# Performance work log

Measured on AMD Instinct MI355X. Metric: run time of the kernel, lower is better.

## Reference

```python
import jax, jax.numpy as jnp
import numpy as np

DIMS = 1024
HEAD = 16
HEAD_DIM = DIMS // HEAD  # 64
BASE_THETA = 10000.0


def setup_inputs() -> dict:
    key = jax.random.key(0)
    ks = jax.random.split(key, 8)
    B, S = 2, 2048
    x = jax.random.normal(ks[0], (B, S, DIMS), dtype=jnp.float32)
    # causal additive mask (use -1e9 instead of -inf for finite grads)
    mask = jnp.where(jnp.tril(jnp.ones((S, S), dtype=bool)), 0.0, -1e9).astype(jnp.float32)
    init = 0.02
    Wq = jax.random.normal(ks[1], (DIMS, DIMS), dtype=jnp.float32) * init
    bq = jnp.zeros((DIMS,), dtype=jnp.float32)
    Wk = jax.random.normal(ks[2], (DIMS, DIMS), dtype=jnp.float32) * init  # no bias
    Wv = jax.random.normal(ks[3], (DIMS, DIMS), dtype=jnp.float32) * init
    bv = jnp.zeros((DIMS,), dtype=jnp.float32)
    Wo = jax.random.normal(ks[4], (DIMS, DIMS), dtype=jnp.float32) * init
    bo = jnp.zeros((DIMS,), dtype=jnp.float32)
    # learned rotary frequencies, initialized exactly as the torch module
    inv_freq = (1.0 / (BASE_THETA ** (jnp.arange(0, HEAD_DIM, 2, dtype=jnp.float32) / HEAD_DIM))).astype(jnp.float32)
    return {"x": x, "mask": mask, "Wq": Wq, "bq": bq, "Wk": Wk, "Wv": Wv,
            "bv": bv, "Wo": Wo, "bo": bo, "inv_freq": inv_freq}


def _apply_rotary(x, cos, sin):
    # x: [B,H,S,D] with D == 2 * len(inv_freq); cos/sin: [S, D/2]
    xr = x.reshape(*x.shape[:-1], -1, 2)  # [B,H,S,D/2,2]
    a, b = xr[..., 0], xr[..., 1]
    ra = a * cos - b * sin
    rb = a * sin + b * cos
    return jnp.stack([ra, rb], axis=-1).reshape(x.shape)


def reference(x, mask, Wq, bq, Wk, Wv, bv, Wo, bo, inv_freq):
    B, S, D = x.shape
    H, hd = HEAD, HEAD_DIM
    q = jnp.einsum('bsd,ed->bse', x, Wq) + bq
    k = jnp.einsum('bsd,ed->bse', x, Wk)
    v = jnp.einsum('bsd,ed->bse', x, Wv) + bv
    # [B,S,D] -> [B,H,S,hd]
    q = q.reshape(B, S, H, hd).transpose(0, 2, 1, 3)
    k = k.reshape(B, S, H, hd).transpose(0, 2, 1, 3)
    v = v.reshape(B, S, H, hd).transpose(0, 2, 1, 3)
    # rotary embeddings (complex mul expressed with cos/sin)
    t = jnp.arange(S, dtype=jnp.float32)
    freqs = t[:, None] * inv_freq[None, :]  # [S, hd/2]
    cos, sin = jnp.cos(freqs), jnp.sin(freqs)
    q = _apply_rotary(q, cos, sin)
    k = _apply_rotary(k, cos, sin)
    scale = hd ** (-0.25)
    qk = jnp.einsum('bhqd,bhkd->bhqk', q * scale, k * scale)
    qk = qk + mask[:S, :S]
    qk = qk.astype(jnp.float32)
    w = jax.nn.softmax(qk, axis=-1)  # dropout is identity in eval mode
    out = jnp.einsum('bhqk,bhkd->bhqd', w, v)
    out = out.transpose(0, 2, 1, 3).reshape(B, S, D)
    out = jnp.einsum('bsd,ed->bse', out, Wo) + bo
    return (out, qk)
```

## Files before the change

### kernel.cpp

```cpp
#include <hip/hip_runtime.h>

typedef __attribute__((ext_vector_type(8))) short short8;
typedef __attribute__((ext_vector_type(4))) float floatx4;
typedef unsigned short ushort_t;

static __device__ __forceinline__ ushort_t f2bf(float f) {
  union { float f; unsigned u; } v; v.f = f;
  unsigned r = v.u + 0x7fffu + ((v.u >> 16) & 1u);
  return (ushort_t)(r >> 16);
}
static __device__ __forceinline__ float bf2f(ushort_t s) {
  union { unsigned u; float f; } v; v.u = ((unsigned)s) << 16; return v.f;
}

__global__ void conv_kernel(const float* __restrict__ src, ushort_t* __restrict__ dst, int n) {
  int i = (blockIdx.x * blockDim.x + threadIdx.x) * 4;
  if (i >= n) return;
  float4 f = *(const float4*)(src + i);
  ushort4 u;
  u.x = f2bf(f.x); u.y = f2bf(f.y); u.z = f2bf(f.z); u.w = f2bf(f.w);
  *(ushort4*)(dst + i) = u;
}

__global__ void biascat_kernel(const float* __restrict__ bq, const float* __restrict__ bv,
                               float* __restrict__ bcat) {
  int i = blockIdx.x * blockDim.x + threadIdx.x;
  float v = 0.f;
  if (i < 1024) v = bq[i];
  else if (i >= 2048) v = bv[i - 2048];
  bcat[i] = v;
}

__global__ __launch_bounds__(256) void gemm_bt(
    const ushort_t* __restrict__ A, const ushort_t* __restrict__ Bm,
    const float* __restrict__ bias, float* __restrict__ Cf,
    ushort_t* __restrict__ Cb, int M, int N, int K)
{
  __shared__ ushort_t As[128 * 72];
  __shared__ ushort_t Bs[128 * 72];
  const int tid = threadIdx.x;
  const int wave = tid >> 6, lane = tid & 63;
  const int wm = wave >> 1, wn = wave & 1;
  const int lane15 = lane & 15, quad = lane >> 4;
  const int m0 = blockIdx.y * 128, n0 = blockIdx.x * 128;
  const int lrow = tid >> 3;
  const int lcol = (tid & 7) * 8;

  floatx4 acc[4][4];
#pragma unroll
  for (int a = 0; a < 4; ++a)
#pragma unroll
    for (int b = 0; b < 4; ++b) acc[a][b] = (floatx4){0.f, 0.f, 0.f, 0.f};

  for (int k0 = 0; k0 < K; k0 += 64) {
    __syncthreads();
#pragma unroll
    for (int l = 0; l < 4; ++l) {
      int row = l * 32 + lrow;
      *(short8*)(&As[row * 72 + lcol]) = *(const short8*)(A + (size_t)(m0 + row) * K + k0 + lcol);
      *(short8*)(&Bs[row * 72 + lcol]) = *(const short8*)(Bm + (size_t)(n0 + row) * K + k0 + lcol);
    }
    __syncthreads();
#pragma unroll
    for (int ks = 0; ks < 64; ks += 32) {
      short8 af[4], bf[4];
#pragma unroll
      for (int mi = 0; mi < 4; ++mi)
        af[mi] = *(const short8*)(&As[(wm * 64 + mi * 16 + lane15) * 72 + ks + quad * 8]);
#pragma unroll
      for (int ni = 0; ni < 4; ++ni)
        bf[ni] = *(const short8*)(&Bs[(wn * 64 + ni * 16 + lane15) * 72 + ks + quad * 8]);
#pragma unroll
      for (int mi = 0; mi < 4; ++mi)
#pragma unroll
        for (int ni = 0; ni < 4; ++ni)
          acc[mi][ni] = __builtin_amdgcn_mfma_f32_16x16x32_bf16(af[mi], bf[ni], acc[mi][ni], 0, 0, 0);
    }
  }

#pragma unroll
  for (int mi = 0; mi < 4; ++mi) {
#pragma unroll
    for (int ni = 0; ni < 4; ++ni) {
      const int col = n0 + wn * 64 + ni * 16 + lane15;
      const float bv = bias ? bias[col] : 0.f;
#pragma unroll
      for (int v = 0; v < 4; ++v) {
        const int row = m0 + wm * 64 + mi * 16 + quad * 4 + v;
        const float val = acc[mi][ni][v] + bv;
        if (Cf) Cf[(size_t)row * N + col] = val;
        else    Cb[(size_t)row * N + col] = f2bf(val);
      }
    }
  }
}

__global__ void rotary_kernel(ushort_t* __restrict__ qkv, const float* __restrict__ inv_freq,
                              int colbase) {
  int tid = blockIdx.x * blockDim.x + threadIdx.x;
  int f = tid & 31;
  int h = (tid >> 5) & 15;
  int s = (tid >> 9) & 2047;
  int b = tid >> 20;
  size_t idx = (size_t)(b * 2048 + s) * 3072 + colbase + h * 64 + 2 * f;
  float ang = (float)s * inv_freq[f];
  float sn, cs;
  sincosf(ang, &sn, &cs);
  float a = bf2f(qkv[idx]);
  float bb = bf2f(qkv[idx + 1]);
  qkv[idx]     = f2bf(a * cs - bb * sn);
  qkv[idx + 1] = f2bf(a * sn + bb * cs);
}

__global__ void transpose_v_kernel(const ushort_t* __restrict__ QKV, ushort_t* __restrict__ VtG) {
  int g = blockIdx.x * blockDim.x + threadIdx.x;
  int s = g & 2047;
  int dchunk = (g >> 11) & 7;
  int bh = g >> 14;
  int b = bh >> 4, h = bh & 15;
  short8 v = *(const short8*)(QKV + (size_t)(b * 2048 + s) * 3072 + 2048 + h * 64 + dchunk * 8);
  ushort_t* dst = VtG + (size_t)bh * 64 * 2048 + (size_t)dchunk * 8 * 2048 + s;
#pragma unroll
  for (int e = 0; e < 8; ++e) dst[(size_t)e * 2048] = (ushort_t)v[e];
}

__global__ void fill_kernel(float* __restrict__ qk_out) {
  const int tile = blockIdx.x;
  const int it = tile >> 4, jt = tile & 15;
  if (jt <= it) return;
  const float4 val = {-1e9f, -1e9f, -1e9f, -1e9f};
  float* base = qk_out + (size_t)blockIdx.y * 2048 * 2048 + (size_t)it * 128 * 2048 + jt * 128;
#pragma unroll
  for (int l = 0; l < 16; ++l) {
    int idx = l * 256 + threadIdx.x;
    int row = idx >> 5, c4 = (idx & 31) * 4;
    *(float4*)(base + (size_t)row * 2048 + c4) = val;
  }
}

__global__ __launch_bounds__(256) void flash_kernel(
    const ushort_t* __restrict__ QKV, const ushort_t* __restrict__ VtG,
    float* __restrict__ qk_out, ushort_t* __restrict__ AO)
{
  __shared__ ushort_t Ps[4][32 * 136];
  const int tid = threadIdx.x;
  const int w = tid >> 6, lane = tid & 63;
  const int lane15 = lane & 15, quad = lane >> 4;
  const int it = 15 - blockIdx.x;
  const int bh = blockIdx.y;
  const int b = bh >> 4, h = bh & 15;
  const int i_base = it * 128 + w * 32;
  const size_t srow0 = (size_t)b * 2048;

  short8 aq[2][2];
#pragma unroll
  for (int mi = 0; mi < 2; ++mi)
#pragma unroll
    for (int kb = 0; kb < 2; ++kb)
      aq[mi][kb] = *(const short8*)(QKV + (srow0 + i_base + mi * 16 + lane15) * 3072
                                    + h * 64 + kb * 32 + quad * 8);

  float mrow[2][4], lrow[2][4];
  floatx4 o[2][4];
#pragma unroll
  for (int mi = 0; mi < 2; ++mi) {
#pragma unroll
    for (int v = 0; v < 4; ++v) { mrow[mi][v] = -3.0e38f; lrow[mi][v] = 0.f; }
#pragma unroll
    for (int nd = 0; nd < 4; ++nd) o[mi][nd] = (floatx4){0.f, 0.f, 0.f, 0.f};
  }

  float* qk_bh = qk_out + (size_t)bh * 2048 * 2048;
  const ushort_t* Vt_bh = VtG + (size_t)bh * 64 * 2048;

  for (int jt = 0; jt <= it; ++jt) {
    const int j0 = jt * 128;

    floatx4 s[2][8];
#pragma unroll
    for (int mi = 0; mi < 2; ++mi)
#pragma unroll
      for (int ni = 0; ni < 8; ++ni) s[mi][ni] = (floatx4){0.f, 0.f, 0.f, 0.f};
#pragma unroll
    for (int ni = 0; ni < 8; ++ni) {
#pragma unroll
      for (int kb = 0; kb < 2; ++kb) {
        short8 bk = *(const short8*)(QKV + (srow0 + j0 + ni * 16 + lane15) * 3072
                                     + 1024 + h * 64 + kb * 32 + quad * 8);
        s[0][ni] = __builtin_amdgcn_mfma_f32_16x16x32_bf16(aq[0][kb], bk, s[0][ni], 0, 0, 0);
        s[1][ni] = __builtin_amdgcn_mfma_f32_16x16x32_bf16(aq[1][kb], bk, s[1][ni], 0, 0, 0);
      }
    }

    float nm[2][4];
#pragma unroll
    for (int mi = 0; mi < 2; ++mi)
#pragma unroll
      for (int v = 0; v < 4; ++v) nm[mi][v] = mrow[mi][v];
#pragma unroll
    for (int mi = 0; mi < 2; ++mi) {
#pragma unroll
      for (int ni = 0; ni < 8; ++ni) {
        const int j_g = j0 + ni * 16 + lane15;
#pragma unroll
        for (int v = 0; v < 4; ++v) {
          const int i_g = i_base + mi * 16 + quad * 4 + v;
          float val = s[mi][ni][v] * 0.125f + ((j_g <= i_g) ? 0.f : -1e9f);
          s[mi][ni][v] = val;
          qk_bh[(size_t)i_g * 2048 + j_g] = val;
          nm[mi][v] = fmaxf(nm[mi][v], val);
        }
      }
    }
#pragma unroll
    for (int mi = 0; mi < 2; ++mi)
#pragma unroll
      for (int v = 0; v < 4; ++v) {
#pragma unroll
        for (int off = 1; off < 16; off <<= 1)
          nm[mi][v] = fmaxf(nm[mi][v], __shfl_xor(nm[mi][v], off));
      }

    float alpha[2][4], rs[2][4];
#pragma unroll
    for (int mi = 0; mi < 2; ++mi)
#pragma unroll
      for (int v = 0; v < 4; ++v) {
        alpha[mi][v] = __expf(mrow[mi][v] - nm[mi][v]);
        rs[mi][v] = 0.f;
      }
#pragma unroll
    for (int mi = 0; mi < 2; ++mi)
#pragma unroll
      for (int ni = 0; ni < 8; ++ni)
#pragma unroll
        for (int v = 0; v < 4; ++v) {
          float p = __expf(s[mi][ni][v] - nm[mi][v]);
          rs[mi][v] += p;
          Ps[w][(mi * 16 + quad * 4 + v) * 136 + ni * 16 + lane15] = f2bf(p);
        }
#pragma unroll
    for (int mi = 0; mi < 2; ++mi)
#pragma unroll
      for (int v = 0; v < 4; ++v) {
#pragma unroll
        for (int off = 1; off < 16; off <<= 1)
          rs[mi][v] += __shfl_xor(rs[mi][v], off);
        lrow[mi][v] = lrow[mi][v] * alpha[mi][v] + rs[mi][v];
        mrow[mi][v] = nm[mi][v];
      }
#pragma unroll
    for (int mi = 0; mi < 2; ++mi)
#pragma unroll
      for (int nd = 0; nd < 4; ++nd)
#pragma unroll
        for (int v = 0; v < 4; ++v) o[mi][nd][v] *= alpha[mi][v];

#pragma unroll
    for (int kb2 = 0; kb2 < 4; ++kb2) {
      short8 ap0 = *(const short8*)&Ps[w][(lane15) * 136 + kb2 * 32 + quad * 8];
      short8 ap1 = *(const short8*)&Ps[w][(16 + lane15) * 136 + kb2 * 32 + quad * 8];
#pragma unroll
      for (int nd = 0; nd < 4; ++nd) {
        short8 bv = *(const short8*)(Vt_bh + (size_t)(nd * 16 + lane15) * 2048
                                     + j0 + kb2 * 32 + quad * 8);
        o[0][nd] = __builtin_amdgcn_mfma_f32_16x16x32_bf16(ap0, bv, o[0][nd], 0, 0, 0);
        o[1][nd] = __builtin_amdgcn_mfma_f32_16x16x32_bf16(ap1, bv, o[1][nd], 0, 0, 0);
      }
    }
  }

#pragma unroll
  for (int mi = 0; mi < 2; ++mi) {
    float inv[4];
#pragma unroll
    for (int v = 0; v < 4; ++v) inv[v] = 1.f / lrow[mi][v];
#pragma unroll
    for (int nd = 0; nd < 4; ++nd)
#pragma unroll
      for (int v = 0; v < 4; ++v) {
        const int i_g = i_base + mi * 16 + quad * 4 + v;
        AO[(srow0 + i_g) * 1024 + h * 64 + nd * 16 + lane15] = f2bf(o[mi][nd][v] * inv[v]);
      }
  }
}

extern "C" void kernel_launch(void* const* d_in, const int* in_sizes, int n_in,
                              void* d_out, int out_size, void* d_ws, size_t ws_size,
                              hipStream_t stream) {
  const float* x  = (const float*)d_in[0];
  const float* Wq = (const float*)d_in[2];
  const float* bq = (const float*)d_in[3];
  const float* Wk = (const float*)d_in[4];
  const float* Wv = (const float*)d_in[5];
  const float* bv = (const float*)d_in[6];
  const float* Wo = (const float*)d_in[7];
  const float* bo = (const float*)d_in[8];
  const float* inv_freq = (const float*)d_in[9];

  char* ws = (char*)d_ws;
  ushort_t* xb   = (ushort_t*)(ws);
  ushort_t* vtg  = (ushort_t*)(ws);
  ushort_t* wb   = (ushort_t*)(ws + ((size_t)8  << 20));
  float*    bcat = (float*)   (ws + ((size_t)16 << 20));
  ushort_t* qkv  = (ushort_t*)(ws + ((size_t)17 << 20));
  ushort_t* aob  = (ushort_t*)(ws + ((size_t)41 << 20));

  float* out0  = (float*)d_out;
  float* qkout = out0 + 4194304;

  conv_kernel<<<4096, 256, 0, stream>>>(x, xb, 4194304);
  conv_kernel<<<1024, 256, 0, stream>>>(Wq, wb,           1048576);
  conv_kernel<<<1024, 256, 0, stream>>>(Wk, wb + 1048576, 1048576);
  conv_kernel<<<1024, 256, 0, stream>>>(Wv, wb + 2097152, 1048576);
  conv_kernel<<<1024, 256, 0, stream>>>(Wo, wb + 3145728, 1048576);
  biascat_kernel<<<12, 256, 0, stream>>>(bq, bv, bcat);

  gemm_bt<<<dim3(24, 32), 256, 0, stream>>>(xb, wb, bcat, nullptr, qkv, 4096, 3072, 1024);

  rotary_kernel<<<8192, 256, 0, stream>>>(qkv, inv_freq, 0);
  rotary_kernel<<<8192, 256, 0, stream>>>(qkv, inv_freq, 1024);

  transpose_v_kernel<<<2048, 256, 0, stream>>>(qkv, vtg);

  fill_kernel<<<dim3(256, 32), 256, 0, stream>>>(qkout);

  flash_kernel<<<dim3(16, 32), 256, 0, stream>>>(qkv, vtg, qkout, aob);

  gemm_bt<<<dim3(8, 32), 256, 0, stream>>>(aob, wb + 3145728, bo, out0, nullptr, 4096, 1024, 1024);
}
```

Before: 1.007 ms.

## Split flash attention into score, stats-reduce and PV kernels over triangular tiles

Replaces the single flash kernel, which had 16 query-tile blocks per head with very uneven causal work, with three kernels. A score kernel launches one block per lower-triangular tile and writes qk plus per-tile row max and sum. A stats kernel merges these into a final max and inverse sum, and a PV kernel re-reads the fp32 scores from global memory, exponentiates them and multiplies by V, pairing short and long query rows to balance work. This improves parallelism and load balance but adds a full re-read of the score matrix and extra launches, and the pstats buffer aliases the aob workspace region.

New measurement: 949.2 us. 1.06x faster.

```diff
diff --git a/kernel.cpp b/kernel.cpp
--- a/kernel.cpp
+++ b/kernel.cpp
@@ -12,6 +12,8 @@
 static __device__ __forceinline__ float bf2f(ushort_t s) {
   union { unsigned u; float f; } v; v.u = ((unsigned)s) << 16; return v.f;
 }
+
+#define L2E 1.4426950408889634f
 
 __global__ void conv_kernel(const float* __restrict__ src, ushort_t* __restrict__ dst, int n) {
   int i = (blockIdx.x * blockDim.x + threadIdx.x) * 4;
@@ -138,18 +140,24 @@
   }
 }
 
-__global__ __launch_bounds__(256) void flash_kernel(
-    const ushort_t* __restrict__ QKV, const ushort_t* __restrict__ VtG,
-    float* __restrict__ qk_out, ushort_t* __restrict__ AO)
+__global__ __launch_bounds__(256) void score_kernel(
+    const ushort_t* __restrict__ QKV, float* __restrict__ qk_out,
+    float2* __restrict__ pstats )
 {
-  __shared__ ushort_t Ps[4][32 * 136];
   const int tid = threadIdx.x;
   const int w = tid >> 6, lane = tid & 63;
   const int lane15 = lane & 15, quad = lane >> 4;
-  const int it = 15 - blockIdx.x;
+  const int t = blockIdx.x;
   const int bh = blockIdx.y;
   const int b = bh >> 4, h = bh & 15;
+
+  int it = (int)((sqrtf((float)(8 * t + 1)) - 1.0f) * 0.5f);
+  while ((it + 1) * (it + 2) / 2 <= t) ++it;
+  while (it * (it + 1) / 2 > t) --it;
+  const int jt = t - it * (it + 1) / 2;
+
   const int i_base = it * 128 + w * 32;
+  const int j0 = jt * 128;
   const size_t srow0 = (size_t)b * 2048;
 
   short8 aq[2][2];
@@ -160,127 +168,143 @@
       aq[mi][kb] = *(const short8*)(QKV + (srow0 + i_base + mi * 16 + lane15) * 3072
                                     + h * 64 + kb * 32 + quad * 8);
 
-  float mrow[2][4], lrow[2][4];
-  floatx4 o[2][4];
+  floatx4 s[2][8];
+#pragma unroll
+  for (int mi = 0; mi < 2; ++mi)
+#pragma unroll
+    for (int ni = 0; ni < 8; ++ni) s[mi][ni] = (floatx4){0.f, 0.f, 0.f, 0.f};
+#pragma unroll
+  for (int ni = 0; ni < 8; ++ni) {
+#pragma unroll
+    for (int kb = 0; kb < 2; ++kb) {
+      short8 bk = *(const short8*)(QKV + (srow0 + j0 + ni * 16 + lane15) * 3072
+                                   + 1024 + h * 64 + kb * 32 + quad * 8);
+      s[0][ni] = __builtin_amdgcn_mfma_f32_16x16x32_bf16(aq[0][kb], bk, s[0][ni], 0, 0, 0);
+      s[1][ni] = __builtin_amdgcn_mfma_f32_16x16x32_bf16(aq[1][kb], bk, s[1][ni], 0, 0, 0);
+    }
+  }
+
+  float* qk_bh = qk_out + (size_t)bh * 2048 * 2048;
+
 #pragma unroll
   for (int mi = 0; mi < 2; ++mi) {
 #pragma unroll
-    for (int v = 0; v < 4; ++v) { mrow[mi][v] = -3.0e38f; lrow[mi][v] = 0.f; }
-#pragma unroll
-    for (int nd = 0; nd < 4; ++nd) o[mi][nd] = (floatx4){0.f, 0.f, 0.f, 0.f};
-  }
-
-  float* qk_bh = qk_out + (size_t)bh * 2048 * 2048;
-  const ushort_t* Vt_bh = VtG + (size_t)bh * 64 * 2048;
-
-  for (int jt = 0; jt <= it; ++jt) {
-    const int j0 = jt * 128;
-
-    floatx4 s[2][8];
-#pragma unroll
-    for (int mi = 0; mi < 2; ++mi)
-#pragma unroll
-      for (int ni = 0; ni < 8; ++ni) s[mi][ni] = (floatx4){0.f, 0.f, 0.f, 0.f};
-#pragma unroll
     for (int ni = 0; ni < 8; ++ni) {
-#pragma unroll
-      for (int kb = 0; kb < 2; ++kb) {
-        short8 bk = *(const short8*)(QKV + (srow0 + j0 + ni * 16 + lane15) * 3072
-                                     + 1024 + h * 64 + kb * 32 + quad * 8);
-        s[0][ni] = __builtin_amdgcn_mfma_f32_16x16x32_bf16(aq[0][kb], bk, s[0][ni], 0, 0, 0);
-        s[1][ni] = __builtin_amdgcn_mfma_f32_16x16x32_bf16(aq[1][kb], bk, s[1][ni], 0, 0, 0);
-      }
-    }
-
-    float nm[2][4];
-#pragma unroll
-    for (int mi = 0; mi < 2; ++mi)
-#pragma unroll
-      for (int v = 0; v < 4; ++v) nm[mi][v] = mrow[mi][v];
-#pragma unroll
-    for (int mi = 0; mi < 2; ++mi) {
-#pragma unroll
-      for (int ni = 0; ni < 8; ++ni) {
-        const int j_g = j0 + ni * 16 + lane15;
-#pragma unroll
-        for (int v = 0; v < 4; ++v) {
-          const int i_g = i_base + mi * 16 + quad * 4 + v;
-          float val = s[mi][ni][v] * 0.125f + ((j_g <= i_g) ? 0.f : -1e9f);
-          s[mi][ni][v] = val;
-          qk_bh[(size_t)i_g * 2048 + j_g] = val;
-          nm[mi][v] = fmaxf(nm[mi][v], val);
-        }
-      }
-    }
-#pragma unroll
-    for (int mi = 0; mi < 2; ++mi)
-#pragma unroll
-      for (int v = 0; v < 4; ++v) {
-#pragma unroll
-        for (int off = 1; off < 16; off <<= 1)
-          nm[mi][v] = fmaxf(nm[mi][v], __shfl_xor(nm[mi][v], off));
-      }
-
-    float alpha[2][4], rs[2][4];
-#pragma unroll
-    for (int mi = 0; mi < 2; ++mi)
-#pragma unroll
-      for (int v = 0; v < 4; ++v) {
-        alpha[mi][v] = __expf(mrow[mi][v] - nm[mi][v]);
-        rs[mi][v] = 0.f;
-      }
-#pragma unroll
-    for (int mi = 0; mi < 2; ++mi)
-#pragma unroll
-      for (int ni = 0; ni < 8; ++ni)
-#pragma unroll
-        for (int v = 0; v < 4; ++v) {
-          float p = __expf(s[mi][ni][v] - nm[mi][v]);
-          rs[mi][v] += p;
-          Ps[w][(mi * 16 + quad * 4 + v) * 136 + ni * 16 + lane15] = f2bf(p);
-        }
-#pragma unroll
-    for (int mi = 0; mi < 2; ++mi)
-#pragma unroll
-      for (int v = 0; v < 4; ++v) {
-#pragma unroll
-        for (int off = 1; off < 16; off <<= 1)
-          rs[mi][v] += __shfl_xor(rs[mi][v], off);
-        lrow[mi][v] = lrow[mi][v] * alpha[mi][v] + rs[mi][v];
-        mrow[mi][v] = nm[mi][v];
-      }
-#pragma unroll
-    for (int mi = 0; mi < 2; ++mi)
-#pragma unroll
-      for (int nd = 0; nd < 4; ++nd)
-#pragma unroll
-        for (int v = 0; v < 4; ++v) o[mi][nd][v] *= alpha[mi][v];
-
-#pragma unroll
-    for (int kb2 = 0; kb2 < 4; ++kb2) {
-      short8 ap0 = *(const short8*)&Ps[w][(lane15) * 136 + kb2 * 32 + quad * 8];
-      short8 ap1 = *(const short8*)&Ps[w][(16 + lane15) * 136 + kb2 * 32 + quad * 8];
-#pragma unroll
-      for (int nd = 0; nd < 4; ++nd) {
-        short8 bv = *(const short8*)(Vt_bh + (size_t)(nd * 16 + lane15) * 2048
-                                     + j0 + kb2 * 32 + quad * 8);
-        o[0][nd] = __builtin_amdgcn_mfma_f32_16x16x32_bf16(ap0, bv, o[0][nd], 0, 0, 0);
-        o[1][nd] = __builtin_amdgcn_mfma_f32_16x16x32_bf16(ap1, bv, o[1][nd], 0, 0, 0);
-      }
-    }
-  }
-
-#pragma unroll
-  for (int mi = 0; mi < 2; ++mi) {
-    float inv[4];
-#pragma unroll
-    for (int v = 0; v < 4; ++v) inv[v] = 1.f / lrow[mi][v];
-#pragma unroll
-    for (int nd = 0; nd < 4; ++nd)
+      const int j_g = j0 + ni * 16 + lane15;
 #pragma unroll
       for (int v = 0; v < 4; ++v) {
         const int i_g = i_base + mi * 16 + quad * 4 + v;
-        AO[(srow0 + i_g) * 1024 + h * 64 + nd * 16 + lane15] = f2bf(o[mi][nd][v] * inv[v]);
+        float val = s[mi][ni][v] * 0.125f + ((j_g <= i_g) ? 0.f : -1e9f);
+        s[mi][ni][v] = val;
+        qk_bh[(size_t)i_g * 2048 + j_g] = val;
+      }
+    }
+  }
+
+#pragma unroll
+  for (int mi = 0; mi < 2; ++mi) {
+#pragma unroll
+    for (int v = 0; v < 4; ++v) {
+      float mv = -3.0e38f;
+#pragma unroll
+      for (int ni = 0; ni < 8; ++ni) mv = fmaxf(mv, s[mi][ni][v]);
+#pragma unroll
+      for (int off = 1; off < 16; off <<= 1)
+        mv = fmaxf(mv, __shfl_xor(mv, off));
+      float ls = 0.f;
+#pragma unroll
+      for (int ni = 0; ni < 8; ++ni)
+        ls += exp2f((s[mi][ni][v] - mv) * L2E);
+#pragma unroll
+      for (int off = 1; off < 16; off <<= 1)
+        ls += __shfl_xor(ls, off);
+      if (lane15 == 0) {
+        const int i_g = i_base + mi * 16 + quad * 4 + v;
+        pstats[(size_t)(bh * 2048 + i_g) * 16 + jt] = make_float2(mv, ls);
+      }
+    }
+  }
+}
+
+__global__ void stats_kernel(const float2* __restrict__ pstats, float2* __restrict__ fstats) {
+  int r = blockIdx.x * blockDim.x + threadIdx.x;
+  int i = r & 2047;
+  int nt = (i >> 7) + 1;
+  const float2* p = pstats + (size_t)r * 16;
+  float m = -3.0e38f;
+  for (int t = 0; t < nt; ++t) m = fmaxf(m, p[t].x);
+  float l = 0.f;
+  for (int t = 0; t < nt; ++t) l += p[t].y * exp2f((p[t].x - m) * L2E);
+  fstats[r] = make_float2(m, 1.f / l);
+}
+
+__global__ __launch_bounds__(256) void pv_kernel(
+    const float* __restrict__ qk, const ushort_t* __restrict__ VtG,
+    const float2* __restrict__ fstats, ushort_t* __restrict__ AO)
+{
+  const int tid = threadIdx.x;
+  const int w = tid >> 6, lane = tid & 63;
+  const int lane15 = lane & 15, quad = lane >> 4;
+  const int wid = blockIdx.x * 4 + w;
+  const int bh = wid >> 6, p = wid & 63;
+  const int b = bh >> 4, h = bh & 15;
+
+  const float* qk_bh = qk + (size_t)bh * 2048 * 2048;
+  const ushort_t* Vt_bh = VtG + (size_t)bh * 64 * 2048;
+  const float2* fs = fstats + (size_t)bh * 2048;
+
+#pragma unroll
+  for (int half = 0; half < 2; ++half) {
+    const int s16 = half ? (127 - p) : p;
+    const int i0 = s16 * 16;
+    const int njt = (s16 >> 3) + 1;
+    const float mr = fs[i0 + lane15].x;
+
+    floatx4 o[4];
+#pragma unroll
+    for (int nd = 0; nd < 4; ++nd) o[nd] = (floatx4){0.f, 0.f, 0.f, 0.f};
+
+    for (int jt = 0; jt < njt; ++jt) {
+      const int j0 = jt * 128;
+      const float* srow = qk_bh + (size_t)(i0 + lane15) * 2048 + j0 + quad * 8;
+
+      short8 ap[4];
+#pragma unroll
+      for (int kb = 0; kb < 4; ++kb) {
+        float4 a0 = *(const float4*)(srow + kb * 32);
+        float4 a1 = *(const float4*)(srow + kb * 32 + 4);
+        short8 a;
+        a[0] = (short)f2bf(exp2f((a0.x - mr) * L2E));
+        a[1] = (short)f2bf(exp2f((a0.y - mr) * L2E));
+        a[2] = (short)f2bf(exp2f((a0.z - mr) * L2E));
+        a[3] = (short)f2bf(exp2f((a0.w - mr) * L2E));
+        a[4] = (short)f2bf(exp2f((a1.x - mr) * L2E));
+        a[5] = (short)f2bf(exp2f((a1.y - mr) * L2E));
+        a[6] = (short)f2bf(exp2f((a1.z - mr) * L2E));
+        a[7] = (short)f2bf(exp2f((a1.w - mr) * L2E));
+        ap[kb] = a;
+      }
+
+#pragma unroll
+      for (int kb = 0; kb < 4; ++kb)
+#pragma unroll
+        for (int nd = 0; nd < 4; ++nd) {
+          short8 bv = *(const short8*)(Vt_bh + (size_t)(nd * 16 + lane15) * 2048
+                                       + j0 + kb * 32 + quad * 8);
+          o[nd] = __builtin_amdgcn_mfma_f32_16x16x32_bf16(ap[kb], bv, o[nd], 0, 0, 0);
+        }
+    }
+
+    float inv[4];
+#pragma unroll
+    for (int v = 0; v < 4; ++v) inv[v] = fs[i0 + quad * 4 + v].y;
+#pragma unroll
+    for (int nd = 0; nd < 4; ++nd)
+#pragma unroll
+      for (int v = 0; v < 4; ++v) {
+        const int i_g = i0 + quad * 4 + v;
+        AO[((size_t)b * 2048 + i_g) * 1024 + h * 64 + nd * 16 + lane15] =
+            f2bf(o[nd][v] * inv[v]);
       }
   }
 }
@@ -303,7 +327,9 @@
   ushort_t* vtg  = (ushort_t*)(ws);
   ushort_t* wb   = (ushort_t*)(ws + ((size_t)8  << 20));
   float*    bcat = (float*)   (ws + ((size_t)16 << 20));
+  float2*   fstats = (float2*)(ws + ((size_t)16 << 20));
   ushort_t* qkv  = (ushort_t*)(ws + ((size_t)17 << 20));
+  float2*   pstats = (float2*)(ws + ((size_t)41 << 20));
   ushort_t* aob  = (ushort_t*)(ws + ((size_t)41 << 20));
 
   float* out0  = (float*)d_out;
@@ -325,7 +351,11 @@
 
   fill_kernel<<<dim3(256, 32), 256, 0, stream>>>(qkout);
 
-  flash_kernel<<<dim3(16, 32), 256, 0, stream>>>(qkv, vtg, qkout, aob);
+  score_kernel<<<dim3(136, 32), 256, 0, stream>>>(qkv, qkout, pstats);
+
+  stats_kernel<<<256, 256, 0, stream>>>(pstats, fstats);
+
+  pv_kernel<<<512, 256, 0, stream>>>(qkout, vtg, fstats, aob);
 
   gemm_bt<<<dim3(8, 32), 256, 0, stream>>>(aob, wb + 3145728, bo, out0, nullptr, 4096, 1024, 1024);
 }
```
